# Kernel optimization log

Hardware: AMD Instinct MI355X
Metric: run time of the kernel (lower is better)

Reference implementation:

```python
import jax, jax.numpy as jnp
import numpy as np

STRIDES = [8, 16, 32, 64, 128]
HW = [(100, 128), (50, 64), (25, 32), (13, 16), (7, 8)]
SCORE_THR = 0.05
IOU_THR = 0.6
MAX_DET = 1000
MAX_OUT = 100  # fixed pad size in _post_process


def _coords(h, w, stride):
    # FCOS coords_fmap2orig: center of each cell in original image coords
    sx = jnp.arange(w, dtype=jnp.float32) * stride + stride // 2
    sy = jnp.arange(h, dtype=jnp.float32) * stride + stride // 2
    yy, xx = jnp.meshgrid(sy, sx, indexing='ij')
    return jnp.stack([xx.reshape(-1), yy.reshape(-1)], axis=-1)  # [h*w, 2]


def _reshape_cat(feats):
    # list of [B,C,h,w] -> [B, sum(h*w), C]
    outs = [f.transpose(0, 2, 3, 1).reshape(f.shape[0], -1, f.shape[1]) for f in feats]
    return jnp.concatenate(outs, axis=1)


def _nms_single(scores, classes, boxes):
    # scores [N] (sorted desc), classes [N] int, boxes [N,4]; greedy DIoU-NMS
    N = scores.shape[0]
    valid = scores >= SCORE_THR
    # batched_nms: offset boxes by class so cross-class boxes never overlap
    max_coord = jnp.max(jnp.where(valid[:, None], boxes, -jnp.inf))
    offs = classes.astype(boxes.dtype) * (max_coord + 1.0)
    b = boxes + offs[:, None]
    x1, y1, x2, y2 = b[:, 0], b[:, 1], b[:, 2], b[:, 3]
    areas = (x2 - x1 + 1.0) * (y2 - y1 + 1.0)
    cx, cy = (x1 + x2) * 0.5, (y1 + y2) * 0.5
    xmin = jnp.maximum(x1[:, None], x1[None, :]); ymin = jnp.maximum(y1[:, None], y1[None, :])
    xmax = jnp.minimum(x2[:, None], x2[None, :]); ymax = jnp.minimum(y2[:, None], y2[None, :])
    inter = jnp.clip(xmax - xmin, 0) * jnp.clip(ymax - ymin, 0)
    iou = inter / (areas[:, None] + areas[None, :] - inter)
    inter_diag = (cx[:, None] - cx[None, :]) ** 2 + (cy[:, None] - cy[None, :]) ** 2
    oxmin = jnp.minimum(x1[:, None], x1[None, :]); oymin = jnp.minimum(y1[:, None], y1[None, :])
    oxmax = jnp.maximum(x2[:, None], x2[None, :]); oymax = jnp.maximum(y2[:, None], y2[None, :])
    outer_diag = (oxmax - oxmin) ** 2 + (oymax - oymin) ** 2
    diou = iou - inter_diag / jnp.maximum(outer_diag, 1e-12)
    idxs = jnp.arange(N)

    def body(i, keep):
        sup = keep[i] & (idxs > i) & (diou[i] > IOU_THR)
        return keep & (~sup)

    keep = jax.lax.fori_loop(0, N, body, valid)
    # kept boxes in descending-score order, padded with -2 to MAX_OUT
    rank = jnp.cumsum(keep) - 1
    pos = jnp.where(keep, jnp.minimum(rank, MAX_OUT), MAX_OUT)  # slot MAX_OUT is dumped
    out_s = jnp.full((MAX_OUT + 1,), -2.0, scores.dtype).at[pos].set(jnp.where(keep, scores, -2.0))[:MAX_OUT]
    out_c = jnp.full((MAX_OUT + 1,), -2, classes.dtype).at[pos].set(jnp.where(keep, classes, -2))[:MAX_OUT]
    out_b = jnp.full((MAX_OUT + 1, 4), -2.0, boxes.dtype).at[pos].set(jnp.where(keep[:, None], boxes, -2.0))[:MAX_OUT]
    return out_s, out_c, out_b


def _forward(cls_feats, reg_feats):
    cls_logits = _reshape_cat(cls_feats)          # [B, L, C]
    reg_preds = _reshape_cat(reg_feats)           # [B, L, 4]
    coords = jnp.concatenate([_coords(h, w, s) for (h, w), s in zip(HW, STRIDES)], axis=0)
    cls_preds = jax.nn.sigmoid(cls_logits)
    cls_scores = jnp.max(cls_preds, axis=-1)      # [B, L]
    cls_classes = jnp.argmax(cls_preds, axis=-1) + 1
    x1y1 = coords[None] - reg_preds[..., :2]
    x2y2 = coords[None] + reg_preds[..., 2:]
    boxes = jnp.concatenate([x1y1, x2y2], axis=-1)  # [B, L, 4]
    max_num = min(MAX_DET, cls_scores.shape[-1])
    topv, topi = jax.lax.top_k(cls_scores, max_num)  # sorted descending
    top_c = jnp.take_along_axis(cls_classes, topi, axis=1)
    top_b = jnp.take_along_axis(boxes, topi[..., None], axis=1)
    return jax.vmap(_nms_single)(topv, top_c, top_b)


def setup_inputs() -> dict:
    key = jax.random.key(0)
    ks = jax.random.split(key, 16)
    inp = {}
    C = 80
    for i, (h, w) in enumerate(HW):
        inp[f'cls{i}'] = jax.random.normal(ks[i], (16, C, h, w), dtype=jnp.float32)
        # ltrb offsets scaled so boxes are realistically sized and overlap
        inp[f'reg{i}'] = jax.random.uniform(ks[5 + i], (16, 4, h, w), dtype=jnp.float32) * 64.0
    inp['boxes_anchor'] = jax.random.normal(ks[10], (16, 100, 4), dtype=jnp.float32)
    inp['labels_anchor'] = jax.random.randint(ks[11], (16, 100), 0, 80)
    inp['score_anchor'] = jax.random.uniform(ks[12], (16, 100), dtype=jnp.float32)
    return inp


def reference(cls0, cls1, cls2, cls3, cls4, reg0, reg1, reg2, reg3, reg4,
              boxes_anchor, labels_anchor, score_anchor):
    # nms_anchor (boxes_anchor, labels_anchor, score_anchor) is consumed but
    # does not affect the output in the original forward.
    scores, classes, boxes = _forward([cls0, cls1, cls2, cls3, cls4],
                                      [reg0, reg1, reg2, reg3, reg4])
    return scores, classes, boxes
```

## Files before the change

### kernel.cpp

```cpp
#include <hip/hip_runtime.h>
#include <math.h>

typedef unsigned int u32;
typedef unsigned long long u64;

#define BB 16
#define NANCH 17064
#define NGRP 4266
#define NTOP 1000
#define NWORD 16
#define NOUT 100
#define NBIN13 8192
#define NSPLIT 17

__device__ __forceinline__ u32 fmap(float v) {
    u32 u = __float_as_uint(v);
    return (u & 0x80000000u) ? ~u : (u | 0x80000000u);
}
__device__ __forceinline__ float funmap(u32 u) {
    u32 b = (u & 0x80000000u) ? (u & 0x7FFFFFFFu) : ~u;
    return __uint_as_float(b);
}

__global__ void __launch_bounds__(256) k_anchor(
        const float* __restrict__ c0, const float* __restrict__ c1,
        const float* __restrict__ c2, const float* __restrict__ c3,
        const float* __restrict__ c4,
        const float* __restrict__ r0, const float* __restrict__ r1,
        const float* __restrict__ r2, const float* __restrict__ r3,
        const float* __restrict__ r4,
        u32* __restrict__ akey, int* __restrict__ aclass,
        float* __restrict__ abox, u32* __restrict__ ghist) {
    __shared__ u32 h1[NBIN13];
    int tid = threadIdx.x;
    int b = blockIdx.y;
    int gt = blockIdx.x * 256 + tid;
    bool valid = gt < 4 * NGRP;

    for (int i = tid; i < NBIN13; i += 256) h1[i] = 0;
    __syncthreads();

    if (valid) {
        int p = gt >> 2, cs = gt & 3;
        int a = p * 4;

        const float *cp, *rp;
        int loc, wl, h, stride, half;
        if (a < 12800)      { loc = a;         wl = 7; h = 100; stride = 8;   half = 4;  cp = c0; rp = r0; }
        else if (a < 16000) { loc = a - 12800; wl = 6; h = 50;  stride = 16;  half = 8;  cp = c1; rp = r1; }
        else if (a < 16800) { loc = a - 16000; wl = 5; h = 25;  stride = 32;  half = 16; cp = c2; rp = r2; }
        else if (a < 17008) { loc = a - 16800; wl = 4; h = 13;  stride = 64;  half = 32; cp = c3; rp = r3; }
        else                { loc = a - 17008; wl = 3; h = 7;   stride = 128; half = 64; cp = c4; rp = r4; }
        int y = loc >> wl, x = loc & ((1 << wl) - 1);
        int hw = h << wl, hwq = hw >> 2;

        const float4* cb4 = (const float4*)(cp + (size_t)b * 80 * hw +
                                            (size_t)cs * 20 * hw + loc);
        float4 buf[20];
#pragma unroll
        for (int c = 0; c < 20; ++c) buf[c] = cb4[(size_t)c * hwq];
        const float4* rb4 = (const float4*)(rp + (size_t)b * 4 * hw + loc);
        float4 gl, gt_, gr, gb;
        if (cs == 0) {
            gl = rb4[0]; gt_ = rb4[hwq]; gr = rb4[2 * hwq]; gb = rb4[3 * hwq];
        }
        __builtin_amdgcn_sched_barrier(0);

        int cbase = cs * 20;
        float m0 = buf[0].x, m1 = buf[0].y, m2 = buf[0].z, m3 = buf[0].w;
        int a0 = cbase, a1 = cbase, a2 = cbase, a3 = cbase;
#pragma unroll
        for (int c = 1; c < 20; ++c) {
            float4 u = buf[c];
            int cc = cbase + c;
            if (u.x > m0) { m0 = u.x; a0 = cc; }
            if (u.y > m1) { m1 = u.y; a1 = cc; }
            if (u.z > m2) { m2 = u.z; a2 = cc; }
            if (u.w > m3) { m3 = u.w; a3 = cc; }
        }
        {
            bool low = (cs & 1) == 0;
            float pm; int pa; bool tk;
            pm = __shfl_xor(m0, 1); pa = __shfl_xor(a0, 1);
            tk = low ? (m0 >= pm) : (m0 > pm); m0 = tk ? m0 : pm; a0 = tk ? a0 : pa;
            pm = __shfl_xor(m1, 1); pa = __shfl_xor(a1, 1);
            tk = low ? (m1 >= pm) : (m1 > pm); m1 = tk ? m1 : pm; a1 = tk ? a1 : pa;
            pm = __shfl_xor(m2, 1); pa = __shfl_xor(a2, 1);
            tk = low ? (m2 >= pm) : (m2 > pm); m2 = tk ? m2 : pm; a2 = tk ? a2 : pa;
            pm = __shfl_xor(m3, 1); pa = __shfl_xor(a3, 1);
            tk = low ? (m3 >= pm) : (m3 > pm); m3 = tk ? m3 : pm; a3 = tk ? a3 : pa;
        }
        {
            bool low = (cs & 2) == 0;
            float pm; int pa; bool tk;
            pm = __shfl_xor(m0, 2); pa = __shfl_xor(a0, 2);
            tk = low ? (m0 >= pm) : (m0 > pm); m0 = tk ? m0 : pm; a0 = tk ? a0 : pa;
            pm = __shfl_xor(m1, 2); pa = __shfl_xor(a1, 2);
            tk = low ? (m1 >= pm) : (m1 > pm); m1 = tk ? m1 : pm; a1 = tk ? a1 : pa;
            pm = __shfl_xor(m2, 2); pa = __shfl_xor(a2, 2);
            tk = low ? (m2 >= pm) : (m2 > pm); m2 = tk ? m2 : pm; a2 = tk ? a2 : pa;
            pm = __shfl_xor(m3, 2); pa = __shfl_xor(a3, 2);
            tk = low ? (m3 >= pm) : (m3 > pm); m3 = tk ? m3 : pm; a3 = tk ? a3 : pa;
        }
        if (cs == 0) {
            int idx = b * NANCH + a;
            u32 km0 = fmap(m0), km1 = fmap(m1), km2 = fmap(m2), km3 = fmap(m3);
            *(uint4*)(akey + idx) = make_uint4(km0, km1, km2, km3);
            *(int4*)(aclass + idx) = make_int4(a0 + 1, a1 + 1, a2 + 1, a3 + 1);
            atomicAdd(&h1[km0 >> 19], 1u);
            atomicAdd(&h1[km1 >> 19], 1u);
            atomicAdd(&h1[km2 >> 19], 1u);
            atomicAdd(&h1[km3 >> 19], 1u);
            float cy = (float)(y * stride + half);
            float cx0 = (float)(x * stride + half);
            float gls[4] = {gl.x, gl.y, gl.z, gl.w};
            float gts[4] = {gt_.x, gt_.y, gt_.z, gt_.w};
            float grs[4] = {gr.x, gr.y, gr.z, gr.w};
            float gbs[4] = {gb.x, gb.y, gb.z, gb.w};
#pragma unroll
            for (int k = 0; k < 4; ++k) {
                float cx = cx0 + (float)(k * stride);
                *(float4*)(abox + (size_t)(idx + k) * 4) =
                    make_float4(cx - gls[k], cy - gts[k], cx + grs[k], cy + gbs[k]);
            }
        }
    }
    __syncthreads();
    u32* gh = ghist + (size_t)b * NBIN13;
    for (int i = tid; i < NBIN13; i += 256) {
        u32 c = h1[i];
        if (c) atomicAdd(&gh[i], c);
    }
}

__global__ void __launch_bounds__(256) k_compact(const u32* __restrict__ akey,
                                                 const u32* __restrict__ ghist,
                                                 u32* __restrict__ ccnt,
                                                 u64* __restrict__ cand) {
    __shared__ u32 seg[256];
    __shared__ u32 binb[32];
    __shared__ int Gs;
    __shared__ u32 thrS;
    __shared__ u32 lcnt, baseoff;
    int b = blockIdx.y, s = blockIdx.x, t = threadIdx.x;
    const u32* gh = ghist + (size_t)b * NBIN13;

    u32 sum = 0;
    {
        const uint4* g4 = (const uint4*)(gh + t * 32);
#pragma unroll
        for (int j = 0; j < 8; ++j) {
            uint4 q = g4[j];
            sum += q.x + q.y + q.z + q.w;
        }
    }
    seg[t] = sum;
    if (t == 0) { Gs = 0; lcnt = 0; }
    __syncthreads();
    for (int off = 1; off < 256; off <<= 1) {
        u32 v = seg[t];
        u32 add = (t + off < 256) ? seg[t + off] : 0u;
        __syncthreads();
        seg[t] = v + add;
        __syncthreads();
    }
    if (seg[t] >= NTOP) atomicMax(&Gs, t);
    __syncthreads();
    int G = Gs;
    u32 hi = (G < 255) ? seg[G + 1] : 0u;
    if (t < 32) binb[t] = gh[G * 32 + t];
    __syncthreads();
    if (t == 0) {
        u32 acc = hi;
        int T13 = G * 32;
        for (int i = 31; i >= 0; --i) {
            acc += binb[i];
            if (acc >= NTOP) { T13 = G * 32 + i; break; }
        }
        thrS = (u32)T13;
    }
    __syncthreads();
    u32 T = thrS;

    int base = s * 1024;
    int n = min(1024, NANCH - base);
    u32 kk[4]; u32 pos[4]; bool m[4] = {false, false, false, false};
    if (4 * t < n) {
        uint4 k4 = *(const uint4*)(akey + (size_t)b * NANCH + base + 4 * t);
        kk[0] = k4.x; kk[1] = k4.y; kk[2] = k4.z; kk[3] = k4.w;
#pragma unroll
        for (int i = 0; i < 4; ++i) {
            m[i] = (kk[i] >> 19) >= T;
            if (m[i]) pos[i] = atomicAdd(&lcnt, 1u);
        }
    }
    __syncthreads();
    if (t == 0) baseoff = atomicAdd(&ccnt[b], lcnt);
    __syncthreads();
    u32 bo = baseoff;
    u64* cb = cand + (size_t)b * NANCH;
#pragma unroll
    for (int i = 0; i < 4; ++i) {
        if (m[i])
            cb[bo + pos[i]] =
                ((u64)kk[i] << 32) | (u64)(0xFFFFFFFFu - (u32)(base + 4 * t + i));
    }
}

__global__ void __launch_bounds__(256) k_rank(
        const u64* __restrict__ cand, const u32* __restrict__ ccnt,
        const int* __restrict__ aclass, const float* __restrict__ abox,
        float* __restrict__ tscore, int* __restrict__ tclass,
        float* __restrict__ tbox, u32* __restrict__ maxcU) {
    __shared__ u64 tile[2048];
    int b = blockIdx.y, tid = threadIdx.x;
    int C = (int)ccnt[b];
    const u64* ck = cand + (size_t)b * NANCH;
    for (int base = blockIdx.x * 256; base < C; base += gridDim.x * 256) {
        int i = base + tid;
        bool have = i < C;
        u64 my = have ? ck[i] : 0ull;
        int rank = 0;
        for (int t0 = 0; t0 < C; t0 += 2048) {
            int nt = min(2048, C - t0);
            __syncthreads();
            for (int j = tid; j < nt; j += 256) tile[j] = ck[t0 + j];
            __syncthreads();
            int q0 = 0, q1 = 0, q2 = 0, q3 = 0, q4 = 0, q5 = 0, q6 = 0, q7 = 0;
            int j = 0;
            for (; j + 8 <= nt; j += 8) {
                u64 v0 = tile[j + 0], v1 = tile[j + 1];
                u64 v2 = tile[j + 2], v3 = tile[j + 3];
                u64 v4 = tile[j + 4], v5 = tile[j + 5];
                u64 v6 = tile[j + 6], v7 = tile[j + 7];
                q0 += v0 > my; q1 += v1 > my; q2 += v2 > my; q3 += v3 > my;
                q4 += v4 > my; q5 += v5 > my; q6 += v6 > my; q7 += v7 > my;
            }
            for (; j < nt; ++j) q0 += tile[j] > my;
            rank += ((q0 + q1) + (q2 + q3)) + ((q4 + q5) + (q6 + q7));
        }
        u32 mymax = 0;
        if (have && rank < NTOP) {
            u32 a = 0xFFFFFFFFu - (u32)(my & 0xFFFFFFFFull);
            int src = b * NANCH + (int)a;
            int dst = b * NTOP + rank;
            float logit = funmap((u32)(my >> 32));
            float sc = 1.0f / (1.0f + expf(-logit));
            float b0 = abox[src * 4 + 0], b1 = abox[src * 4 + 1];
            float b2 = abox[src * 4 + 2], b3 = abox[src * 4 + 3];
            tscore[dst] = sc;
            tclass[dst] = aclass[src];
            tbox[dst * 4 + 0] = b0;
            tbox[dst * 4 + 1] = b1;
            tbox[dst * 4 + 2] = b2;
            tbox[dst * 4 + 3] = b3;
            if (sc >= 0.05f)
                mymax = fmap(fmaxf(fmaxf(b0, b1), fmaxf(b2, b3)));
        }
        for (int off = 32; off > 0; off >>= 1) {
            u32 o = (u32)__shfl_down((int)mymax, off);
            mymax = mymax > o ? mymax : o;
        }
        if ((tid & 63) == 0) atomicMax(&maxcU[b], mymax);
    }
}

__global__ void k_sup(const float* __restrict__ tbox, const int* __restrict__ tclass,
                      const u32* __restrict__ maxcU, u64* __restrict__ sup) {
    int u = blockIdx.x, b = blockIdx.y;
    int ti = 0, rem = u;
    while (rem >= NWORD - ti) { rem -= NWORD - ti; ++ti; }
    int tj = ti + rem;
    int t = threadIdx.x;
    __shared__ double jx1[64], jy1[64], jx2[64], jy2[64], jcx[64], jcy[64], jar[64];
    double mc1 = (double)funmap(maxcU[b]) + 1.0;
    int j = tj * 64 + t;
    if (j < NTOP) {
        const float* bx = tbox + (size_t)(b * NTOP + j) * 4;
        double o = (double)tclass[b * NTOP + j] * mc1;
        double x1 = (double)bx[0] + o, y1 = (double)bx[1] + o;
        double x2 = (double)bx[2] + o, y2 = (double)bx[3] + o;
        jx1[t] = x1; jy1[t] = y1; jx2[t] = x2; jy2[t] = y2;
        jcx[t] = (x1 + x2) * 0.5; jcy[t] = (y1 + y2) * 0.5;
        jar[t] = (x2 - x1 + 1.0) * (y2 - y1 + 1.0);
    }
    __syncthreads();
    int i = ti * 64 + t;
    if (i >= NTOP) return;
    const float* bx = tbox + (size_t)(b * NTOP + i) * 4;
    double o = (double)tclass[b * NTOP + i] * mc1;
    double ix1 = (double)bx[0] + o, iy1 = (double)bx[1] + o;
    double ix2 = (double)bx[2] + o, iy2 = (double)bx[3] + o;
    double icx = (ix1 + ix2) * 0.5, icy = (iy1 + iy2) * 0.5;
    double iar = (ix2 - ix1 + 1.0) * (iy2 - iy1 + 1.0);
    u64 bits = 0;
    int jbase = tj * 64;
    for (int jj = 0; jj < 64; ++jj) {
        int jg = jbase + jj;
        if (jg >= NTOP) break;
        if (jg <= i) continue;
        double xm = fmax(ix1, jx1[jj]), ym = fmax(iy1, jy1[jj]);
        double xM = fmin(ix2, jx2[jj]), yM = fmin(iy2, jy2[jj]);
        double inter = fmax(xM - xm, 0.0) * fmax(yM - ym, 0.0);
        double U = iar + jar[jj] - inter;
        double dx = icx - jcx[jj], dy = icy - jcy[jj];
        double idg = dx * dx + dy * dy;
        double ox = fmax(ix2, jx2[jj]) - fmin(ix1, jx1[jj]);
        double oy = fmax(iy2, jy2[jj]) - fmin(iy1, jy1[jj]);
        double odg = fmax(ox * ox + oy * oy, 1e-12);
        if (inter * odg - idg * U > 0.6 * (U * odg)) bits |= (1ull << jj);
    }
    sup[(size_t)(b * NTOP + i) * NWORD + tj] = bits;
}

__global__ void __launch_bounds__(256) k_scan(
        const u64* __restrict__ sup, const float* __restrict__ tscore,
        const int* __restrict__ tclass, const float* __restrict__ tbox,
        float* __restrict__ out) {
    int b = blockIdx.x, tid = threadIdx.x;
    int lane = tid & 63;
    __shared__ u64 tl[2][64 * 17];
    __shared__ float sc_s[1024];
    __shared__ int kept_lds[NOUT];
    __shared__ int kept_sh;
    const u64* supb = sup + (size_t)b * NTOP * NWORD;
    for (int i = tid; i < 1024; i += 256)
        sc_s[i] = (i < NTOP) ? tscore[b * NTOP + i] : -1.0f;
    if (tid == 0) kept_sh = 0;
    for (int q = 0; q < 4; ++q) {
        int e = q * 256 + tid;
        int rr = e >> 4, w = e & 15;
        tl[0][rr * 17 + w] = (rr < NTOP) ? supb[(size_t)rr * 16 + w] : 0ull;
    }
    __syncthreads();
    u64 remw = 0;
    int kept = 0;
    for (int t = 0; t < NWORD; ++t) {
        int cur = t & 1;
        if (tid >= 64) {
            if (t + 1 < NWORD) {
                int r1 = (t + 1) * 64;
                for (int e = tid - 64; e < 1024; e += 192) {
                    int rr = r1 + (e >> 4), w = e & 15;
                    tl[cur ^ 1][(e >> 4) * 17 + w] =
                        (rr < NTOP) ? supb[(size_t)rr * 16 + w] : 0ull;
                }
            }
        } else {
            int r0 = t * 64;
            int r = r0 + lane;
            float s = sc_s[r];
            u64 vmask = __ballot(s >= 0.05f);
            u64 M = tl[cur][lane * 17 + t];
            u64 rem_t = __shfl(remw, t);
            u64 cnd = vmask & ~rem_t;
            u64 keepmask = 0;
            while (cnd) {
                int k = __ffsll(cnd) - 1;
                keepmask |= 1ull << k;
                if (lane == 0) kept_lds[kept] = r0 + k;
                ++kept;
                if (kept >= NOUT) break;
                u64 Mk = __shfl(M, k);
                cnd &= ~(Mk | (1ull << k));
            }
            if (lane < NWORD) {
                u64 km = keepmask;
                while (km) {
                    int k = __ffsll(km) - 1;
                    km &= km - 1;
                    remw |= tl[cur][k * 17 + lane];
                }
            }
            if (lane == 0) kept_sh = kept;
        }
        __syncthreads();
        if (kept_sh >= NOUT) break;
    }
    float* os = out + b * NOUT;
    float* oc = out + BB * NOUT + b * NOUT;
    float* ob = out + 2 * BB * NOUT + (size_t)b * NOUT * 4;
    for (int i = tid; i < NOUT; i += 256) { os[i] = -2.0f; oc[i] = -2.0f; }
    for (int i = tid; i < NOUT * 4; i += 256) ob[i] = -2.0f;
    __syncthreads();
    int ncopy = kept_sh < NOUT ? kept_sh : NOUT;
    for (int r = tid; r < ncopy; r += 256) {
        int i = kept_lds[r];
        os[r] = tscore[b * NTOP + i];
        oc[r] = (float)tclass[b * NTOP + i];
        ob[r * 4 + 0] = tbox[(size_t)(b * NTOP + i) * 4 + 0];
        ob[r * 4 + 1] = tbox[(size_t)(b * NTOP + i) * 4 + 1];
        ob[r * 4 + 2] = tbox[(size_t)(b * NTOP + i) * 4 + 2];
        ob[r * 4 + 3] = tbox[(size_t)(b * NTOP + i) * 4 + 3];
    }
}

extern "C" void kernel_launch(void* const* d_in, const int* in_sizes, int n_in,
                              void* d_out, int out_size, void* d_ws, size_t ws_size,
                              hipStream_t stream) {
    (void)in_sizes; (void)n_in; (void)out_size; (void)ws_size;
    const float* cls[5];
    const float* reg[5];
    for (int i = 0; i < 5; ++i) {
        cls[i] = (const float*)d_in[2 * i];
        reg[i] = (const float*)d_in[2 * i + 1];
    }
    float* out = (float*)d_out;

    char* ws = (char*)d_ws;
    u32* ghist = (u32*)ws;           ws += (size_t)BB * NBIN13 * sizeof(u32);
    u32* ccnt = (u32*)ws;            ws += 64;
    u32* maxcU = (u32*)ws;           ws += 64;
    size_t zbytes = (size_t)BB * NBIN13 * sizeof(u32) + 128;
    u64* cand = (u64*)ws;            ws += (size_t)BB * NANCH * sizeof(u64);
    u64* sup = (u64*)ws;             ws += (size_t)BB * NTOP * NWORD * sizeof(u64);
    u32* akey = (u32*)ws;            ws += (size_t)BB * NANCH * sizeof(u32);
    int* aclass = (int*)ws;          ws += (size_t)BB * NANCH * sizeof(int);
    float* abox = (float*)ws;        ws += (size_t)BB * NANCH * 4 * sizeof(float);
    float* tscore = (float*)ws;      ws += (size_t)BB * NTOP * sizeof(float);
    int* tclass = (int*)ws;          ws += (size_t)BB * NTOP * sizeof(int);
    float* tbox = (float*)ws;        ws += (size_t)BB * NTOP * 4 * sizeof(float);

    hipMemsetAsync(ghist, 0, zbytes, stream);

    k_anchor<<<dim3((4 * NGRP + 255) / 256, BB), 256, 0, stream>>>(
        cls[0], cls[1], cls[2], cls[3], cls[4],
        reg[0], reg[1], reg[2], reg[3], reg[4],
        akey, aclass, abox, ghist);
    k_compact<<<dim3(NSPLIT, BB), 256, 0, stream>>>(akey, ghist, ccnt, cand);
    k_rank<<<dim3(14, BB), 256, 0, stream>>>(cand, ccnt, aclass, abox,
                                             tscore, tclass, tbox, maxcU);
    k_sup<<<dim3(136, BB), 64, 0, stream>>>(tbox, tclass, maxcU, sup);
    k_scan<<<BB, 256, 0, stream>>>(sup, tscore, tclass, tbox, out);
}
```

Baseline: 217.7 us.

## Fuse candidate compaction into rank kernel with per-block LDS candidate list

Merges k_compact and k_rank into one kernel. Each of the 17 blocks per image independently rescans all anchor keys, builds the full thresholded candidate list in shared memory via a prefix-sum compaction, then ranks its slice against that LDS copy. This removes one launch, the global candidate buffer and counter, and the atomic-based compaction, but every block redoes the key scan and compaction. Candidates beyond a fixed LDS cap of 6144 are silently dropped.

```diff
diff --git a/kernel.cpp b/kernel.cpp
--- a/kernel.cpp
+++ b/kernel.cpp
@@ -12,6 +12,7 @@
 #define NOUT 100
 #define NBIN13 8192
 #define NSPLIT 17
+#define CANDCAP 6144
 
 __device__ __forceinline__ u32 fmap(float v) {
     u32 u = __float_as_uint(v);
@@ -133,17 +134,19 @@
     }
 }
 
-__global__ void __launch_bounds__(256) k_compact(const u32* __restrict__ akey,
-                                                 const u32* __restrict__ ghist,
-                                                 u32* __restrict__ ccnt,
-                                                 u64* __restrict__ cand) {
+__global__ void __launch_bounds__(256) k_rank(
+        const u32* __restrict__ akey, const u32* __restrict__ ghist,
+        const int* __restrict__ aclass, const float* __restrict__ abox,
+        float* __restrict__ tscore, int* __restrict__ tclass,
+        float* __restrict__ tbox, u32* __restrict__ maxcU) {
+    __shared__ u64 cand[CANDCAP];
     __shared__ u32 seg[256];
     __shared__ u32 binb[32];
     __shared__ int Gs;
     __shared__ u32 thrS;
-    __shared__ u32 lcnt, baseoff;
     int b = blockIdx.y, s = blockIdx.x, t = threadIdx.x;
     const u32* gh = ghist + (size_t)b * NBIN13;
+    const uint4* ak4 = (const uint4*)(akey + (size_t)b * NANCH);
 
     u32 sum = 0;
     {
@@ -155,7 +158,7 @@
         }
     }
     seg[t] = sum;
-    if (t == 0) { Gs = 0; lcnt = 0; }
+    if (t == 0) Gs = 0;
     __syncthreads();
     for (int off = 1; off < 256; off <<= 1) {
         u32 v = seg[t];
@@ -182,63 +185,58 @@
     __syncthreads();
     u32 T = thrS;
 
-    int base = s * 1024;
-    int n = min(1024, NANCH - base);
-    u32 kk[4]; u32 pos[4]; bool m[4] = {false, false, false, false};
-    if (4 * t < n) {
-        uint4 k4 = *(const uint4*)(akey + (size_t)b * NANCH + base + 4 * t);
-        kk[0] = k4.x; kk[1] = k4.y; kk[2] = k4.z; kk[3] = k4.w;
+    u32 cnt = 0;
+    for (int i = t; i < NGRP; i += 256) {
+        uint4 k4 = ak4[i];
+        cnt += (k4.x >> 19) >= T;
+        cnt += (k4.y >> 19) >= T;
+        cnt += (k4.z >> 19) >= T;
+        cnt += (k4.w >> 19) >= T;
+    }
+    __syncthreads();
+    seg[t] = cnt;
+    __syncthreads();
+    for (int off = 1; off < 256; off <<= 1) {
+        u32 v = seg[t];
+        u32 add = (t >= off) ? seg[t - off] : 0u;
+        __syncthreads();
+        seg[t] = v + add;
+        __syncthreads();
+    }
+    u32 pos = seg[t] - cnt;
+    int C = (int)seg[255];
+    if (C > CANDCAP) C = CANDCAP;
+    for (int i = t; i < NGRP; i += 256) {
+        uint4 k4 = ak4[i];
+        u32 kk[4] = {k4.x, k4.y, k4.z, k4.w};
 #pragma unroll
-        for (int i = 0; i < 4; ++i) {
-            m[i] = (kk[i] >> 19) >= T;
-            if (m[i]) pos[i] = atomicAdd(&lcnt, 1u);
-        }
-    }
-    __syncthreads();
-    if (t == 0) baseoff = atomicAdd(&ccnt[b], lcnt);
-    __syncthreads();
-    u32 bo = baseoff;
-    u64* cb = cand + (size_t)b * NANCH;
-#pragma unroll
-    for (int i = 0; i < 4; ++i) {
-        if (m[i])
-            cb[bo + pos[i]] =
-                ((u64)kk[i] << 32) | (u64)(0xFFFFFFFFu - (u32)(base + 4 * t + i));
-    }
-}
-
-__global__ void __launch_bounds__(256) k_rank(
-        const u64* __restrict__ cand, const u32* __restrict__ ccnt,
-        const int* __restrict__ aclass, const float* __restrict__ abox,
-        float* __restrict__ tscore, int* __restrict__ tclass,
-        float* __restrict__ tbox, u32* __restrict__ maxcU) {
-    __shared__ u64 tile[2048];
-    int b = blockIdx.y, tid = threadIdx.x;
-    int C = (int)ccnt[b];
-    const u64* ck = cand + (size_t)b * NANCH;
-    for (int base = blockIdx.x * 256; base < C; base += gridDim.x * 256) {
-        int i = base + tid;
+        for (int jj = 0; jj < 4; ++jj) {
+            if ((kk[jj] >> 19) >= T) {
+                if (pos < CANDCAP)
+                    cand[pos] = ((u64)kk[jj] << 32) |
+                                (u64)(0xFFFFFFFFu - (u32)(4 * i + jj));
+                ++pos;
+            }
+        }
+    }
+    __syncthreads();
+
+    for (int base = s * 256; base < C; base += NSPLIT * 256) {
+        int i = base + t;
         bool have = i < C;
-        u64 my = have ? ck[i] : 0ull;
-        int rank = 0;
-        for (int t0 = 0; t0 < C; t0 += 2048) {
-            int nt = min(2048, C - t0);
-            __syncthreads();
-            for (int j = tid; j < nt; j += 256) tile[j] = ck[t0 + j];
-            __syncthreads();
-            int q0 = 0, q1 = 0, q2 = 0, q3 = 0, q4 = 0, q5 = 0, q6 = 0, q7 = 0;
-            int j = 0;
-            for (; j + 8 <= nt; j += 8) {
-                u64 v0 = tile[j + 0], v1 = tile[j + 1];
-                u64 v2 = tile[j + 2], v3 = tile[j + 3];
-                u64 v4 = tile[j + 4], v5 = tile[j + 5];
-                u64 v6 = tile[j + 6], v7 = tile[j + 7];
-                q0 += v0 > my; q1 += v1 > my; q2 += v2 > my; q3 += v3 > my;
-                q4 += v4 > my; q5 += v5 > my; q6 += v6 > my; q7 += v7 > my;
-            }
-            for (; j < nt; ++j) q0 += tile[j] > my;
-            rank += ((q0 + q1) + (q2 + q3)) + ((q4 + q5) + (q6 + q7));
-        }
+        u64 my = have ? cand[i] : 0ull;
+        int q0 = 0, q1 = 0, q2 = 0, q3 = 0, q4 = 0, q5 = 0, q6 = 0, q7 = 0;
+        int j = 0;
+        for (; j + 8 <= C; j += 8) {
+            u64 v0 = cand[j + 0], v1 = cand[j + 1];
+            u64 v2 = cand[j + 2], v3 = cand[j + 3];
+            u64 v4 = cand[j + 4], v5 = cand[j + 5];
+            u64 v6 = cand[j + 6], v7 = cand[j + 7];
+            q0 += v0 > my; q1 += v1 > my; q2 += v2 > my; q3 += v3 > my;
+            q4 += v4 > my; q5 += v5 > my; q6 += v6 > my; q7 += v7 > my;
+        }
+        for (; j < C; ++j) q0 += cand[j] > my;
+        int rank = ((q0 + q1) + (q2 + q3)) + ((q4 + q5) + (q6 + q7));
         u32 mymax = 0;
         if (have && rank < NTOP) {
             u32 a = 0xFFFFFFFFu - (u32)(my & 0xFFFFFFFFull);
@@ -261,7 +259,7 @@
             u32 o = (u32)__shfl_down((int)mymax, off);
             mymax = mymax > o ? mymax : o;
         }
-        if ((tid & 63) == 0) atomicMax(&maxcU[b], mymax);
+        if ((t & 63) == 0) atomicMax(&maxcU[b], mymax);
     }
 }
 
@@ -409,10 +407,8 @@
 
     char* ws = (char*)d_ws;
     u32* ghist = (u32*)ws;           ws += (size_t)BB * NBIN13 * sizeof(u32);
-    u32* ccnt = (u32*)ws;            ws += 64;
     u32* maxcU = (u32*)ws;           ws += 64;
-    size_t zbytes = (size_t)BB * NBIN13 * sizeof(u32) + 128;
-    u64* cand = (u64*)ws;            ws += (size_t)BB * NANCH * sizeof(u64);
+    size_t zbytes = (size_t)BB * NBIN13 * sizeof(u32) + 64;
     u64* sup = (u64*)ws;             ws += (size_t)BB * NTOP * NWORD * sizeof(u64);
     u32* akey = (u32*)ws;            ws += (size_t)BB * NANCH * sizeof(u32);
     int* aclass = (int*)ws;          ws += (size_t)BB * NANCH * sizeof(int);
@@ -427,9 +423,8 @@
         cls[0], cls[1], cls[2], cls[3], cls[4],
         reg[0], reg[1], reg[2], reg[3], reg[4],
         akey, aclass, abox, ghist);
-    k_compact<<<dim3(NSPLIT, BB), 256, 0, stream>>>(akey, ghist, ccnt, cand);
-    k_rank<<<dim3(14, BB), 256, 0, stream>>>(cand, ccnt, aclass, abox,
-                                             tscore, tclass, tbox, maxcU);
+    k_rank<<<dim3(NSPLIT, BB), 256, 0, stream>>>(akey, ghist, aclass, abox,
+                                                 tscore, tclass, tbox, maxcU);
     k_sup<<<dim3(136, BB), 64, 0, stream>>>(tbox, tclass, maxcU, sup);
     k_scan<<<BB, 256, 0, stream>>>(sup, tscore, tclass, tbox, out);
 }
```

Measured after the change: 218.1 us. About the same (+0.2%).

## Split class argmax across 8 lanes and pack shared histogram into byte counters

Applied to the files above, without the earlier changes.

Each anchor group is now handled by 8 lanes with 10 classes each instead of 4 lanes with 20, which halves per-thread register buffers and doubles the grid, adding one more shuffle reduction stage. The per-block LDS histogram packs four 8-bit counters per word, cutting shared memory from 32KB to 8KB and the clearing/flush work, which should raise occupancy. Byte counters are safe because each block now covers only 128 anchors, so no bin can overflow 255. The flush unpacks each word into up to four global atomics.

```diff
diff --git a/kernel.cpp b/kernel.cpp
--- a/kernel.cpp
+++ b/kernel.cpp
@@ -31,17 +31,18 @@
         const float* __restrict__ r4,
         u32* __restrict__ akey, int* __restrict__ aclass,
         float* __restrict__ abox, u32* __restrict__ ghist) {
-    __shared__ u32 h1[NBIN13];
+    __shared__ u32 h8[NBIN13 / 4];
     int tid = threadIdx.x;
     int b = blockIdx.y;
     int gt = blockIdx.x * 256 + tid;
-    bool valid = gt < 4 * NGRP;
-
-    for (int i = tid; i < NBIN13; i += 256) h1[i] = 0;
+    bool valid = gt < 8 * NGRP;
+
+    uint4* hz = (uint4*)h8;
+    for (int i = tid; i < NBIN13 / 16; i += 256) hz[i] = make_uint4(0, 0, 0, 0);
     __syncthreads();
 
     if (valid) {
-        int p = gt >> 2, cs = gt & 3;
+        int p = gt >> 3, cs = gt & 7;
         int a = p * 4;
 
         const float *cp, *rp;
@@ -55,10 +56,10 @@
         int hw = h << wl, hwq = hw >> 2;
 
         const float4* cb4 = (const float4*)(cp + (size_t)b * 80 * hw +
-                                            (size_t)cs * 20 * hw + loc);
-        float4 buf[20];
-#pragma unroll
-        for (int c = 0; c < 20; ++c) buf[c] = cb4[(size_t)c * hwq];
+                                            (size_t)cs * 10 * hw + loc);
+        float4 buf[10];
+#pragma unroll
+        for (int c = 0; c < 10; ++c) buf[c] = cb4[(size_t)c * hwq];
         const float4* rb4 = (const float4*)(rp + (size_t)b * 4 * hw + loc);
         float4 gl, gt_, gr, gb;
         if (cs == 0) {
@@ -66,11 +67,11 @@
         }
         __builtin_amdgcn_sched_barrier(0);
 
-        int cbase = cs * 20;
+        int cbase = cs * 10;
         float m0 = buf[0].x, m1 = buf[0].y, m2 = buf[0].z, m3 = buf[0].w;
         int a0 = cbase, a1 = cbase, a2 = cbase, a3 = cbase;
 #pragma unroll
-        for (int c = 1; c < 20; ++c) {
+        for (int c = 1; c < 10; ++c) {
             float4 u = buf[c];
             int cc = cbase + c;
             if (u.x > m0) { m0 = u.x; a0 = cc; }
@@ -78,28 +79,17 @@
             if (u.z > m2) { m2 = u.z; a2 = cc; }
             if (u.w > m3) { m3 = u.w; a3 = cc; }
         }
-        {
-            bool low = (cs & 1) == 0;
+#pragma unroll
+        for (int st = 1; st <= 4; st <<= 1) {
+            bool low = (cs & st) == 0;
             float pm; int pa; bool tk;
-            pm = __shfl_xor(m0, 1); pa = __shfl_xor(a0, 1);
+            pm = __shfl_xor(m0, st); pa = __shfl_xor(a0, st);
             tk = low ? (m0 >= pm) : (m0 > pm); m0 = tk ? m0 : pm; a0 = tk ? a0 : pa;
-            pm = __shfl_xor(m1, 1); pa = __shfl_xor(a1, 1);
+            pm = __shfl_xor(m1, st); pa = __shfl_xor(a1, st);
             tk = low ? (m1 >= pm) : (m1 > pm); m1 = tk ? m1 : pm; a1 = tk ? a1 : pa;
-            pm = __shfl_xor(m2, 1); pa = __shfl_xor(a2, 1);
+            pm = __shfl_xor(m2, st); pa = __shfl_xor(a2, st);
             tk = low ? (m2 >= pm) : (m2 > pm); m2 = tk ? m2 : pm; a2 = tk ? a2 : pa;
-            pm = __shfl_xor(m3, 1); pa = __shfl_xor(a3, 1);
-            tk = low ? (m3 >= pm) : (m3 > pm); m3 = tk ? m3 : pm; a3 = tk ? a3 : pa;
-        }
-        {
-            bool low = (cs & 2) == 0;
-            float pm; int pa; bool tk;
-            pm = __shfl_xor(m0, 2); pa = __shfl_xor(a0, 2);
-            tk = low ? (m0 >= pm) : (m0 > pm); m0 = tk ? m0 : pm; a0 = tk ? a0 : pa;
-            pm = __shfl_xor(m1, 2); pa = __shfl_xor(a1, 2);
-            tk = low ? (m1 >= pm) : (m1 > pm); m1 = tk ? m1 : pm; a1 = tk ? a1 : pa;
-            pm = __shfl_xor(m2, 2); pa = __shfl_xor(a2, 2);
-            tk = low ? (m2 >= pm) : (m2 > pm); m2 = tk ? m2 : pm; a2 = tk ? a2 : pa;
-            pm = __shfl_xor(m3, 2); pa = __shfl_xor(a3, 2);
+            pm = __shfl_xor(m3, st); pa = __shfl_xor(a3, st);
             tk = low ? (m3 >= pm) : (m3 > pm); m3 = tk ? m3 : pm; a3 = tk ? a3 : pa;
         }
         if (cs == 0) {
@@ -107,10 +97,11 @@
             u32 km0 = fmap(m0), km1 = fmap(m1), km2 = fmap(m2), km3 = fmap(m3);
             *(uint4*)(akey + idx) = make_uint4(km0, km1, km2, km3);
             *(int4*)(aclass + idx) = make_int4(a0 + 1, a1 + 1, a2 + 1, a3 + 1);
-            atomicAdd(&h1[km0 >> 19], 1u);
-            atomicAdd(&h1[km1 >> 19], 1u);
-            atomicAdd(&h1[km2 >> 19], 1u);
-            atomicAdd(&h1[km3 >> 19], 1u);
+            u32 b0 = km0 >> 19, b1 = km1 >> 19, b2 = km2 >> 19, b3 = km3 >> 19;
+            atomicAdd(&h8[b0 >> 2], 1u << ((b0 & 3) << 3));
+            atomicAdd(&h8[b1 >> 2], 1u << ((b1 & 3) << 3));
+            atomicAdd(&h8[b2 >> 2], 1u << ((b2 & 3) << 3));
+            atomicAdd(&h8[b3 >> 2], 1u << ((b3 & 3) << 3));
             float cy = (float)(y * stride + half);
             float cx0 = (float)(x * stride + half);
             float gls[4] = {gl.x, gl.y, gl.z, gl.w};
@@ -127,9 +118,17 @@
     }
     __syncthreads();
     u32* gh = ghist + (size_t)b * NBIN13;
-    for (int i = tid; i < NBIN13; i += 256) {
-        u32 c = h1[i];
-        if (c) atomicAdd(&gh[i], c);
+    for (int i = tid; i < NBIN13 / 4; i += 256) {
+        u32 w = h8[i];
+        if (w) {
+            int b4 = i * 4;
+            u32 c0v = w & 0xFFu, c1v = (w >> 8) & 0xFFu;
+            u32 c2v = (w >> 16) & 0xFFu, c3v = (w >> 24) & 0xFFu;
+            if (c0v) atomicAdd(&gh[b4 + 0], c0v);
+            if (c1v) atomicAdd(&gh[b4 + 1], c1v);
+            if (c2v) atomicAdd(&gh[b4 + 2], c2v);
+            if (c3v) atomicAdd(&gh[b4 + 3], c3v);
+        }
     }
 }
 
@@ -423,7 +422,7 @@
 
     hipMemsetAsync(ghist, 0, zbytes, stream);
 
-    k_anchor<<<dim3((4 * NGRP + 255) / 256, BB), 256, 0, stream>>>(
+    k_anchor<<<dim3((8 * NGRP + 255) / 256, BB), 256, 0, stream>>>(
         cls[0], cls[1], cls[2], cls[3], cls[4],
         reg[0], reg[1], reg[2], reg[3], reg[4],
         akey, aclass, abox, ghist);
```

New measurement: 220.9 us. No clear change (+1.5%).
